# Optimization experiments

Measured on AMD Instinct MI355X. Metric: run time of the kernel, lower is better.

The kernel has to match this reference:

```python
import math
import jax, jax.numpy as jnp
import numpy as np
from jax import lax

B, T, D, S, N_SLOTS, N_ITERS = 16, 4096, 768, 768, 16, 8
THR, EPS = 0.5, 1e-8
SCALE = D ** -0.5
NEG = -jnp.finfo(jnp.float32).max


def ln(x, g, b):
    mu = x.mean(-1, keepdims=True)
    var = ((x - mu) ** 2).mean(-1, keepdims=True)
    return (x - mu) / jnp.sqrt(var + 1e-5) * g + b


def gru_cell(u, h, wih, whh, bih, bhh):
    # torch GRUCell: r,z,n gate ordering
    gi = u @ wih.T + bih
    gh = h @ whh.T + bhh
    ir, iz, inn = jnp.split(gi, 3, axis=-1)
    hr, hz, hn = jnp.split(gh, 3, axis=-1)
    r = jax.nn.sigmoid(ir + hr)
    z = jax.nn.sigmoid(iz + hz)
    n = jnp.tanh(inn + r * hn)
    return (1.0 - z) * n + z * h


def sa_step(slots, k, v, p, slot_mask, context_mask):
    q = ln(slots, p['lsg'], p['lsb']) @ p['Wq'].T
    dots = jnp.einsum('bid,bjd->bij', q, k) * SCALE  # [B, n_slots, T]
    dots = jnp.where(context_mask[:, None, :], dots, NEG)
    if slot_mask is not None:
        dots = jnp.where(slot_mask[:, :, None], dots, NEG)
    attn_vis = jax.nn.softmax(dots, axis=1)  # softmax over SLOTS (inverted attn)
    attn = attn_vis + EPS
    attn = attn / attn.sum(-1, keepdims=True)
    updates = jnp.einsum('bjd,bij->bid', v, attn)
    b, n, d = slots.shape
    h = gru_cell(updates.reshape(b * n, d), slots.reshape(b * n, d),
                 p['gwih'], p['gwhh'], p['gbih'], p['gbhh'])
    slots = h.reshape(b, n, d)
    pre = ln(slots, p['lfg'], p['lfb'])
    slots = slots + (jax.nn.relu(pre @ p['w1'].T + p['b1']) @ p['w2'].T + p['b2'])
    return slots, attn_vis


def cluster_single(slots, attn, slot_mask):
    sl = lax.stop_gradient(slots)  # torch no_grad block
    ns = sl / jnp.clip(jnp.linalg.norm(sl, axis=-1, keepdims=True), 1e-12)
    smm = (slot_mask[:, :, None] & slot_mask[:, None, :]).astype(jnp.float32)
    dist = 1.0 - jnp.einsum('bnd,bmd->bnm', ns, ns)
    dist = jnp.where(smm > 0, dist, 2.0)
    adj = (dist < THR).astype(jnp.float32) * smm
    for _ in range(math.ceil(math.log2(N_SLOTS))):  # transitive closure by squaring
        adj = jnp.minimum(adj @ adj, 1.0) * smm
    cum = jnp.cumsum(adj, axis=1)
    cm = adj * (cum <= 1.0)  # keep first row of each connected component
    counts = (cm > 0).any(axis=2).sum(axis=1)
    reset = counts < 3
    eye = jnp.eye(N_SLOTS, dtype=jnp.float32)[None] * slot_mask[:, :, None].astype(jnp.float32)
    cm = jnp.where(reset[:, None, None], eye, cm)
    cw = cm / jnp.clip(cm.sum(axis=2, keepdims=True), 1.0)
    cm = lax.stop_gradient(cm)
    cw = lax.stop_gradient(cw)
    means = cw @ slots          # grads flow through slots only
    cattn = cm @ attn           # grads flow through attn only
    out_mask = (cm > 0).any(axis=2) & slot_mask
    return means, cattn, out_mask


def setup_inputs() -> dict:
    key = jax.random.key(0)
    ks = jax.random.split(key, 16)
    sc = 0.02
    return {
        'x': jax.random.normal(ks[0], (B, T, D), jnp.float32),
        'context_mask': jnp.ones((B, T), jnp.bool_),
        'n_slots': N_SLOTS,
        'slots_init': jax.random.normal(ks[1], (N_SLOTS, S), jnp.float32),
        'Wk': jax.random.normal(ks[2], (S, D), jnp.float32) * sc,
        'Wv': jax.random.normal(ks[3], (S, D), jnp.float32) * sc,
        'Wq': jax.random.normal(ks[4], (S, S), jnp.float32) * sc,
        'gwih': jax.random.normal(ks[5], (3 * S, S), jnp.float32) * sc,
        'gwhh': jax.random.normal(ks[6], (3 * S, S), jnp.float32) * sc,
        'gbih': jnp.zeros((3 * S,), jnp.float32),
        'gbhh': jnp.zeros((3 * S,), jnp.float32),
        'w1': jax.random.normal(ks[7], (4 * S, S), jnp.float32) * sc,
        'b1': jnp.zeros((4 * S,), jnp.float32),
        'w2': jax.random.normal(ks[8], (S, 4 * S), jnp.float32) * sc,
        'b2': jnp.zeros((S,), jnp.float32),
        'lin_g': jnp.ones((D,), jnp.float32), 'lin_b': jnp.zeros((D,), jnp.float32),
        'lsg': jnp.ones((S,), jnp.float32), 'lsb': jnp.zeros((S,), jnp.float32),
        'lfg': jnp.ones((S,), jnp.float32), 'lfb': jnp.zeros((S,), jnp.float32),
    }


def reference(x, context_mask, n_slots, slots_init, Wk, Wv, Wq, gwih, gwhh,
              gbih, gbhh, w1, b1, w2, b2, lin_g, lin_b, lsg, lsb, lfg, lfb):
    p = dict(Wq=Wq, gwih=gwih, gwhh=gwhh, gbih=gbih, gbhh=gbhh,
             w1=w1, b1=b1, w2=w2, b2=b2, lsg=lsg, lsb=lsb, lfg=lfg, lfb=lfb)
    xn = ln(x, lin_g, lin_b)
    init_slots = jnp.broadcast_to(slots_init[None], (x.shape[0], N_SLOTS, S))
    k = xn @ Wk.T
    v = xn @ Wv.T
    slots = init_slots
    for _ in range(N_ITERS):
        slots, attn = sa_step(slots, k, v, p, None, context_mask)
    # implicit differentiation trick
    slots = lax.stop_gradient(slots) - lax.stop_gradient(init_slots) + init_slots
    slot_mask = jnp.ones((x.shape[0], N_SLOTS), jnp.bool_)
    slots, attn = sa_step(slots, k, v, p, slot_mask, context_mask)
    slots, attn, slot_mask = cluster_single(slots, attn, slot_mask)
    attn_map = jnp.transpose(attn, (0, 2, 1))  # [B, T, n_slots]
    return slots, attn_map, slot_mask
```

## Files before the change

kernel.cpp:

```cpp
#include <hip/hip_runtime.h>
#include <hip/hip_bf16.h>

typedef __hip_bfloat16 bf16;
typedef __attribute__((ext_vector_type(4))) float f32x4;
typedef __attribute__((ext_vector_type(8))) short s16x8;
typedef unsigned int u32;
typedef unsigned short u16;

#define B_ 16
#define T_ 4096
#define D_ 768
#define S_ 768
#define NS 16
#define NIT 9
#define NCHUNK 16
#define TCH 256
#define EPS 1e-8f
#define SCALE 0.036084391824351615f

__device__ __forceinline__ void gld16(const void* g, void* l) {
    __builtin_amdgcn_global_load_lds((const __attribute__((address_space(1))) u32*)g,
                                     (__attribute__((address_space(3))) u32*)l, 16, 0, 0);
}

__device__ __forceinline__ u16 bfbits(float x) {
    bf16 h = __float2bfloat16(x);
    return *reinterpret_cast<u16*>(&h);
}

__global__ void f2bf_kernel(const float* __restrict__ in, bf16* __restrict__ out, int n) {
    int i = blockIdx.x * 256 + threadIdx.x;
    if (i < n) out[i] = __float2bfloat16(in[i]);
}

__global__ void __launch_bounds__(256) ln768_kernel(
    const float* __restrict__ x, const float* __restrict__ g,
    const float* __restrict__ bta, bf16* __restrict__ out)
{
    int row = blockIdx.x;
    int tid = threadIdx.x;
    const float* xr = x + (size_t)row * 768;
    float v0 = xr[tid], v1 = xr[tid + 256], v2 = xr[tid + 512];
    float s = v0 + v1 + v2;
    int lane = tid & 63, wid = tid >> 6;
    #pragma unroll
    for (int off = 32; off; off >>= 1) s += __shfl_down(s, off);
    __shared__ float red[4];
    __shared__ float sh_mu, sh_rs;
    if (lane == 0) red[wid] = s;
    __syncthreads();
    if (tid == 0) sh_mu = (red[0] + red[1] + red[2] + red[3]) * (1.f / 768.f);
    __syncthreads();
    float mu = sh_mu;
    float d0 = v0 - mu, d1 = v1 - mu, d2 = v2 - mu;
    float q = d0 * d0 + d1 * d1 + d2 * d2;
    #pragma unroll
    for (int off = 32; off; off >>= 1) q += __shfl_down(q, off);
    if (lane == 0) red[wid] = q;
    __syncthreads();
    if (tid == 0) sh_rs = rsqrtf((red[0] + red[1] + red[2] + red[3]) * (1.f / 768.f) + 1e-5f);
    __syncthreads();
    float rs = sh_rs;
    bf16* orow = out + (size_t)row * 768;
    orow[tid]       = __float2bfloat16(d0 * rs * g[tid]       + bta[tid]);
    orow[tid + 256] = __float2bfloat16(d1 * rs * g[tid + 256] + bta[tid + 256]);
    orow[tid + 512] = __float2bfloat16(d2 * rs * g[tid + 512] + bta[tid + 512]);
}

__global__ void __launch_bounds__(256) gemm128_kernel(
    const bf16* __restrict__ A, const bf16* __restrict__ Bm, bf16* __restrict__ Cb,
    int M, int N, int K)
{
    __shared__ bf16 As[128 * 64];
    __shared__ bf16 Bs[128 * 64];
    int tid = threadIdx.x, lane = tid & 63, wid = tid >> 6;
    int bm0 = blockIdx.x * 128, bn0 = blockIdx.y * 128;
    int wr = wid >> 1, wc = wid & 1;
    int g = lane >> 4, r15 = lane & 15;
    const f32x4 vzero = {0.f, 0.f, 0.f, 0.f};
    f32x4 acc[4][4];
    #pragma unroll
    for (int m = 0; m < 4; ++m)
        #pragma unroll
        for (int n = 0; n < 4; ++n) acc[m][n] = vzero;

    for (int kt = 0; kt < K; kt += 64) {
        __syncthreads();
        #pragma unroll
        for (int i = 0; i < 4; ++i) {
            int sa = wid * 64 + i * 256;
            int o = (sa + lane) * 16;
            int r = o >> 7, cb = o & 127;
            int cbs = cb ^ ((r & 7) << 4);
            gld16(A + (size_t)(bm0 + r) * K + kt + (cbs >> 1), (char*)As + (size_t)sa * 16);
        }
        #pragma unroll
        for (int i = 0; i < 4; ++i) {
            int sa = wid * 64 + i * 256;
            int o = (sa + lane) * 16;
            int r = o >> 7, cb = o & 127;
            int cbs = cb ^ ((r & 7) << 4);
            gld16(Bm + (size_t)(bn0 + r) * K + kt + (cbs >> 1), (char*)Bs + (size_t)sa * 16);
        }
        asm volatile("s_waitcnt vmcnt(0)" ::: "memory");
        __syncthreads();
        #pragma unroll
        for (int kk = 0; kk < 64; kk += 32) {
            s16x8 af[4], bfr[4];
            #pragma unroll
            for (int m = 0; m < 4; ++m) {
                int r = wr * 64 + m * 16 + r15;
                int p = r * 128 + ((kk * 2 + g * 16) ^ ((r & 7) << 4));
                af[m] = *(const s16x8*)((const char*)As + p);
            }
            #pragma unroll
            for (int n = 0; n < 4; ++n) {
                int r = wc * 64 + n * 16 + r15;
                int p = r * 128 + ((kk * 2 + g * 16) ^ ((r & 7) << 4));
                bfr[n] = *(const s16x8*)((const char*)Bs + p);
            }
            #pragma unroll
            for (int m = 0; m < 4; ++m)
                #pragma unroll
                for (int n = 0; n < 4; ++n)
                    acc[m][n] = __builtin_amdgcn_mfma_f32_16x16x32_bf16(af[m], bfr[n], acc[m][n], 0, 0, 0);
        }
    }
    #pragma unroll
    for (int m = 0; m < 4; ++m) {
        int cm = bm0 + wr * 64 + m * 16 + g * 4;
        #pragma unroll
        for (int n = 0; n < 4; ++n) {
            int cn = bn0 + wc * 64 + n * 16 + r15;
            #pragma unroll
            for (int j = 0; j < 4; ++j)
                Cb[(size_t)(cm + j) * N + cn] = __float2bfloat16(acc[m][n][j]);
        }
    }
}

__global__ void __launch_bounds__(256) gemm_skinny_kernel(
    const bf16* __restrict__ A, const bf16* __restrict__ Bm,
    const float* __restrict__ bias, float* __restrict__ Cf, bf16* __restrict__ Cb,
    int M, int N, int K, int relu, int addC)
{
    __shared__ bf16 As[16 * 64];
    __shared__ bf16 Bs[64 * 64];
    int tid = threadIdx.x, lane = tid & 63, wid = tid >> 6;
    int bm0 = blockIdx.x * 16, bn0 = blockIdx.y * 64;
    int g = lane >> 4, r15 = lane & 15;
    const f32x4 vzero = {0.f, 0.f, 0.f, 0.f};
    f32x4 acc = vzero;
    for (int kt = 0; kt < K; kt += 64) {
        __syncthreads();
        #pragma unroll
        for (int i = 0; i < 3; ++i) {
            int s0 = i * 256 + wid * 64;
            if (s0 < 640) {
                int o = (s0 + lane) * 16;
                if (o < 2048) {
                    int r = o >> 7, cb = o & 127;
                    int cbs = cb ^ ((r & 7) << 4);
                    gld16(A + (size_t)(bm0 + r) * K + kt + (cbs >> 1), (char*)As + (size_t)s0 * 16);
                } else {
                    int ob = o - 2048;
                    int r = ob >> 7, cb = ob & 127;
                    int cbs = cb ^ ((r & 7) << 4);
                    gld16(Bm + (size_t)(bn0 + r) * K + kt + (cbs >> 1),
                          (char*)Bs + (size_t)(s0 * 16 - 2048));
                }
            }
        }
        asm volatile("s_waitcnt vmcnt(0)" ::: "memory");
        __syncthreads();
        #pragma unroll
        for (int kk = 0; kk < 64; kk += 32) {
            int ra = r15;
            int pa = ra * 128 + ((kk * 2 + g * 16) ^ ((ra & 7) << 4));
            s16x8 af = *(const s16x8*)((const char*)As + pa);
            int rb = wid * 16 + r15;
            int pb = rb * 128 + ((kk * 2 + g * 16) ^ ((rb & 7) << 4));
            s16x8 bfr = *(const s16x8*)((const char*)Bs + pb);
            acc = __builtin_amdgcn_mfma_f32_16x16x32_bf16(af, bfr, acc, 0, 0, 0);
        }
    }
    int cn = bn0 + wid * 16 + r15;
    float bv = bias ? bias[cn] : 0.f;
    #pragma unroll
    for (int j = 0; j < 4; ++j) {
        int cm = bm0 + g * 4 + j;
        size_t ci = (size_t)cm * N + cn;
        float val = acc[j] + bv;
        if (addC) val += Cf[ci];
        if (relu) val = fmaxf(val, 0.f);
        if (Cf) Cf[ci] = val;
        if (Cb) Cb[ci] = __float2bfloat16(val);
    }
}

__global__ void __launch_bounds__(256) transpose_kernel(
    const bf16* __restrict__ v, bf16* __restrict__ vt)
{
    __shared__ bf16 tile[32][33];
    int b = blockIdx.z;
    int t0 = blockIdx.x * 32, d0 = blockIdx.y * 32;
    int tx = threadIdx.x & 31, ty = threadIdx.x >> 5;
    const bf16* vb = v + (size_t)b * T_ * S_;
    bf16* vtb = vt + (size_t)b * S_ * T_;
    #pragma unroll
    for (int r = ty; r < 32; r += 8)
        tile[r][tx] = vb[(size_t)(t0 + r) * S_ + d0 + tx];
    __syncthreads();
    #pragma unroll
    for (int r = ty; r < 32; r += 8)
        vtb[(size_t)(d0 + r) * T_ + t0 + tx] = tile[tx][r];
}

__global__ void __launch_bounds__(256) vsum_kernel(
    const bf16* __restrict__ vT, float* __restrict__ vsum)
{
    int row = blockIdx.x * 4 + (threadIdx.x >> 6);
    int lane = threadIdx.x & 63;
    const bf16* p = vT + (size_t)row * T_;
    float s = 0.f;
    for (int t = lane * 8; t < T_; t += 64 * 8) {
        s16x8 v8 = *(const s16x8*)(p + t);
        #pragma unroll
        for (int j = 0; j < 8; ++j) {
            union { u32 i; float f; } c;
            c.i = ((u32)(u16)v8[j]) << 16;
            s += c.f;
        }
    }
    #pragma unroll
    for (int off = 32; off; off >>= 1) s += __shfl_down(s, off);
    if (lane == 0) vsum[row] = s;
}

__global__ void init_slots_kernel(const float* __restrict__ si,
                                  float* __restrict__ slots, bf16* __restrict__ slots_bf)
{
    int idx = blockIdx.x * 256 + threadIdx.x;
    float v = si[idx % (NS * S_)];
    slots[idx] = v;
    slots_bf[idx] = __float2bfloat16(v);
}

__global__ void __launch_bounds__(256) fused_attn_kernel(
    const bf16* __restrict__ q_bf, const bf16* __restrict__ k_bf, const bf16* __restrict__ vT,
    float* __restrict__ pU, float* __restrict__ prs, float* __restrict__ avis, int write_avis)
{
    __shared__ bf16 qs[16 * 768];
    __shared__ bf16 ks[32 * 768];
    __shared__ bf16 vs[768 * 32];
    __shared__ bf16 as_[16 * 32];
    __shared__ float rsw[2][16];
    int tid = threadIdx.x, lane = tid & 63, wid = tid >> 6;
    int b = blockIdx.x >> 4, chunk = blockIdx.x & 15;
    int t0 = chunk * TCH;
    int g = lane >> 4, s15 = lane & 15;
    const bf16* qb  = q_bf + (size_t)(b * 16) * 768;
    const bf16* kb  = k_bf + (size_t)b * T_ * 768;
    const bf16* vtb = vT   + (size_t)b * 768 * T_;

    #pragma unroll
    for (int i = 0; i < 6; ++i) {
        int s0 = i * 256 + wid * 64;
        int o = (s0 + lane) * 16;
        int r = o / 1536, cb = o % 1536;
        int cbs = cb ^ ((r & 7) << 4);
        gld16(qb + (size_t)r * 768 + (cbs >> 1), (char*)qs + (size_t)s0 * 16);
    }

    const f32x4 vzero = {0.f, 0.f, 0.f, 0.f};
    f32x4 uacc[12];
    #pragma unroll
    for (int i = 0; i < 12; ++i) uacc[i] = vzero;
    float rs_acc = 0.f;

    for (int ts = 0; ts < TCH / 32; ++ts) {
        int tb = t0 + ts * 32;
        __syncthreads();
        #pragma unroll
        for (int i = 0; i < 12; ++i) {
            int s0 = i * 256 + wid * 64;
            int o = (s0 + lane) * 16;
            int r = o / 1536, cb = o % 1536;
            int cbs = cb ^ ((r & 7) << 4);
            gld16(kb + (size_t)(tb + r) * 768 + (cbs >> 1), (char*)ks + (size_t)s0 * 16);
        }
        #pragma unroll
        for (int i = 0; i < 12; ++i) {
            int s0 = i * 256 + wid * 64;
            int o = (s0 + lane) * 16;
            int d = o >> 6, cb = o & 63;
            int cbs = cb ^ ((d & 3) << 4);
            gld16(vtb + (size_t)d * T_ + tb + (cbs >> 1), (char*)vs + (size_t)s0 * 16);
        }
        asm volatile("s_waitcnt vmcnt(0)" ::: "memory");
        __syncthreads();

        if (wid < 2) {
            f32x4 dacc = vzero;
            #pragma unroll
            for (int kk = 0; kk < 768; kk += 32) {
                int rk = wid * 16 + s15;
                int pk = rk * 1536 + ((kk * 2 + g * 16) ^ ((rk & 7) << 4));
                s16x8 kf = *(const s16x8*)((const char*)ks + pk);
                int pq = s15 * 1536 + ((kk * 2 + g * 16) ^ ((s15 & 7) << 4));
                s16x8 qf = *(const s16x8*)((const char*)qs + pq);
                dacc = __builtin_amdgcn_mfma_f32_16x16x32_bf16(kf, qf, dacc, 0, 0, 0);
            }
            float d0 = dacc[0] * SCALE, d1 = dacc[1] * SCALE,
                  d2 = dacc[2] * SCALE, d3 = dacc[3] * SCALE;
            float m0 = d0, m1 = d1, m2 = d2, m3 = d3;
            #pragma unroll
            for (int off = 1; off < 16; off <<= 1) {
                m0 = fmaxf(m0, __shfl_xor(m0, off));
                m1 = fmaxf(m1, __shfl_xor(m1, off));
                m2 = fmaxf(m2, __shfl_xor(m2, off));
                m3 = fmaxf(m3, __shfl_xor(m3, off));
            }
            float e0 = expf(d0 - m0), e1 = expf(d1 - m1), e2 = expf(d2 - m2), e3 = expf(d3 - m3);
            float q0 = e0, q1 = e1, q2 = e2, q3 = e3;
            #pragma unroll
            for (int off = 1; off < 16; off <<= 1) {
                q0 += __shfl_xor(q0, off);
                q1 += __shfl_xor(q1, off);
                q2 += __shfl_xor(q2, off);
                q3 += __shfl_xor(q3, off);
            }
            float a0 = e0 / q0, a1 = e1 / q1, a2 = e2 / q2, a3 = e3 / q3;
            rs_acc += a0 + a1 + a2 + a3;
            int tl = wid * 16 + g * 4;
            ushort2 p0, p1;
            p0.x = bfbits(a0); p0.y = bfbits(a1);
            p1.x = bfbits(a2); p1.y = bfbits(a3);
            int sw = (s15 & 3) << 4;
            *(ushort2*)((char*)as_ + s15 * 64 + ((tl * 2) ^ sw))       = p0;
            *(ushort2*)((char*)as_ + s15 * 64 + (((tl + 2) * 2) ^ sw)) = p1;
            if (write_avis) {
                f32x4 w = {a0, a1, a2, a3};
                *(f32x4*)(avis + (size_t)(b * 16 + s15) * T_ + tb + tl) = w;
            }
        }
        __syncthreads();
        {
            int pa = s15 * 64 + ((g * 16) ^ ((s15 & 3) << 4));
            s16x8 afr = *(const s16x8*)((const char*)as_ + pa);
            #pragma unroll
            for (int i = 0; i < 12; ++i) {
                int d = (wid * 12 + i) * 16 + s15;
                int pv = d * 64 + ((g * 16) ^ ((d & 3) << 4));
                s16x8 vf = *(const s16x8*)((const char*)vs + pv);
                uacc[i] = __builtin_amdgcn_mfma_f32_16x16x32_bf16(vf, afr, uacc[i], 0, 0, 0);
            }
        }
    }
    float* pUb = pU + (size_t)(b * 16 + chunk) * 768 * 16;
    #pragma unroll
    for (int i = 0; i < 12; ++i) {
        int dbase = (wid * 12 + i) * 16 + g * 4;
        #pragma unroll
        for (int j = 0; j < 4; ++j)
            pUb[(size_t)(dbase + j) * 16 + s15] = uacc[i][j];
    }
    rs_acc += __shfl_xor(rs_acc, 16);
    rs_acc += __shfl_xor(rs_acc, 32);
    if (wid < 2 && lane < 16) rsw[wid][s15] = rs_acc;
    __syncthreads();
    if (tid < 16) prs[(b * 16 + chunk) * 16 + tid] = rsw[0][tid] + rsw[1][tid];
}

__global__ void __launch_bounds__(256) attn_reduce_kernel(
    const float* __restrict__ pU, const float* __restrict__ prs,
    const float* __restrict__ vsum, bf16* __restrict__ upd)
{
    int idx = blockIdx.x * 256 + threadIdx.x;
    int d = idx % 768;
    int s = (idx / 768) & 15;
    int b = idx / (768 * 16);
    float su = 0.f;
    #pragma unroll
    for (int c = 0; c < 16; ++c) su += pU[((size_t)(b * 16 + c) * 768 + d) * 16 + s];
    float rs = 0.f;
    #pragma unroll
    for (int c = 0; c < 16; ++c) rs += prs[(b * 16 + c) * 16 + s];
    float val = (su + EPS * vsum[b * 768 + d]) / (rs + T_ * EPS);
    upd[idx] = __float2bfloat16(val);
}

__global__ void __launch_bounds__(256) gru_gates_kernel(
    const float* __restrict__ gi, const float* __restrict__ gh,
    float* __restrict__ slots, bf16* __restrict__ slots_bf)
{
    int idx = blockIdx.x * 256 + threadIdx.x;
    int r = idx / 768, c = idx - r * 768;
    const float* gir = gi + (size_t)r * 2304;
    const float* ghr = gh + (size_t)r * 2304;
    float ir = gir[c], iz = gir[768 + c], inn = gir[1536 + c];
    float hr = ghr[c], hz = ghr[768 + c], hn  = ghr[1536 + c];
    float rg = 1.f / (1.f + expf(-(ir + hr)));
    float z  = 1.f / (1.f + expf(-(iz + hz)));
    float n  = tanhf(inn + rg * hn);
    float h  = slots[idx];
    float out = (1.f - z) * n + z * h;
    slots[idx] = out;
    slots_bf[idx] = __float2bfloat16(out);
}

__global__ void __launch_bounds__(256) cluster_kernel(
    const float* __restrict__ slots, float* __restrict__ out_slots,
    float* __restrict__ out_mask, float* __restrict__ cm_g)
{
    int b = blockIdx.x;
    __shared__ float s[16][768];
    __shared__ float inv[16];
    __shared__ float adj[16][16], tmp[16][16], cw[16][16];
    __shared__ int reset_s;
    const float* sb = slots + (size_t)b * 16 * 768;
    for (int i = threadIdx.x; i < 16 * 768; i += 256) s[i / 768][i % 768] = sb[i];
    __syncthreads();
    if (threadIdx.x < 16) {
        float q = 0.f;
        for (int d = 0; d < 768; ++d) q += s[threadIdx.x][d] * s[threadIdx.x][d];
        inv[threadIdx.x] = 1.f / fmaxf(sqrtf(q), 1e-12f);
    }
    __syncthreads();
    int n = threadIdx.x >> 4, m = threadIdx.x & 15;
    float dot = 0.f;
    for (int d = 0; d < 768; ++d) dot += s[n][d] * s[m][d];
    dot *= inv[n] * inv[m];
    adj[n][m] = ((1.f - dot) < 0.5f) ? 1.f : 0.f;
    __syncthreads();
    #pragma unroll
    for (int it = 0; it < 4; ++it) {
        float t = 0.f;
        #pragma unroll
        for (int j = 0; j < 16; ++j) t += adj[n][j] * adj[j][m];
        tmp[n][m] = fminf(t, 1.f);
        __syncthreads();
// ... 59 lines not shown
        for (int j = 0; j < 16; ++j) acc += cm[i][j] * avv[j];
        out_attn[((size_t)b * T_ + t) * 16 + i] = acc;
    }
}

extern "C" void kernel_launch(void* const* d_in, const int* in_sizes, int n_in,
                              void* d_out, int out_size, void* d_ws, size_t ws_size,
                              hipStream_t stream)
{
    const float* x    = (const float*)d_in[0];
    const float* si   = (const float*)d_in[3];
    const float* Wk   = (const float*)d_in[4];
    const float* Wv   = (const float*)d_in[5];
    const float* Wq   = (const float*)d_in[6];
    const float* gwih = (const float*)d_in[7];
    const float* gwhh = (const float*)d_in[8];
    const float* gbih = (const float*)d_in[9];
    const float* gbhh = (const float*)d_in[10];
    const float* w1   = (const float*)d_in[11];
    const float* b1   = (const float*)d_in[12];
    const float* w2   = (const float*)d_in[13];
    const float* b2   = (const float*)d_in[14];
    const float* ling = (const float*)d_in[15];
    const float* linb = (const float*)d_in[16];
    const float* lsg  = (const float*)d_in[17];
    const float* lsb  = (const float*)d_in[18];
    const float* lfg  = (const float*)d_in[19];
    const float* lfb  = (const float*)d_in[20];

    char* w = (char*)d_ws;
    size_t off = 0;
    auto alloc = [&](size_t bytes) { void* p = w + off; off += (bytes + 255) & ~(size_t)255; return p; };
    bf16* xn_vt  = (bf16*)alloc((size_t)B_ * T_ * D_ * 2);
    bf16* k_bf   = (bf16*)alloc((size_t)B_ * T_ * S_ * 2);
    bf16* v_bf   = (bf16*)alloc((size_t)B_ * T_ * S_ * 2);
    float* avis  = (float*)alloc((size_t)B_ * NS * T_ * 4);
    float* pU    = (float*)alloc((size_t)B_ * NCHUNK * S_ * NS * 4);
    float* prs   = (float*)alloc((size_t)B_ * NCHUNK * NS * 4);
    float* vsum  = (float*)alloc((size_t)B_ * S_ * 4);
    float* slots = (float*)alloc((size_t)B_ * NS * S_ * 4);
    bf16* slots_bf = (bf16*)alloc((size_t)B_ * NS * S_ * 2);
    bf16* lnsl   = (bf16*)alloc((size_t)B_ * NS * S_ * 2);
    bf16* q_bf   = (bf16*)alloc((size_t)B_ * NS * S_ * 2);
    bf16* upd_bf = (bf16*)alloc((size_t)B_ * NS * S_ * 2);
    float* gi    = (float*)alloc((size_t)B_ * NS * 3 * S_ * 4);
    float* gh    = (float*)alloc((size_t)B_ * NS * 3 * S_ * 4);
    bf16* h1_bf  = (bf16*)alloc((size_t)B_ * NS * 4 * S_ * 2);
    bf16* wq_bf  = (bf16*)alloc((size_t)S_ * S_ * 2);
    bf16* wk_bf  = (bf16*)alloc((size_t)S_ * D_ * 2);
    bf16* wv_bf  = (bf16*)alloc((size_t)S_ * D_ * 2);
    bf16* gwih_bf = (bf16*)alloc((size_t)3 * S_ * S_ * 2);
    bf16* gwhh_bf = (bf16*)alloc((size_t)3 * S_ * S_ * 2);
    bf16* w1_bf  = (bf16*)alloc((size_t)4 * S_ * S_ * 2);
    bf16* w2_bf  = (bf16*)alloc((size_t)S_ * 4 * S_ * 2);
    float* cm_g  = (float*)alloc((size_t)B_ * 256 * 4);

    float* out_slots = (float*)d_out;
    float* out_attn  = out_slots + (size_t)B_ * NS * S_;
    float* out_mask  = out_attn + (size_t)B_ * T_ * NS;

    auto cvt = [&](const float* src, bf16* dst, int n) {
        f2bf_kernel<<<(n + 255) / 256, 256, 0, stream>>>(src, dst, n);
    };
    cvt(Wq, wq_bf, S_ * S_);
    cvt(Wk, wk_bf, S_ * D_);
    cvt(Wv, wv_bf, S_ * D_);
    cvt(gwih, gwih_bf, 3 * S_ * S_);
    cvt(gwhh, gwhh_bf, 3 * S_ * S_);
    cvt(w1, w1_bf, 4 * S_ * S_);
    cvt(w2, w2_bf, S_ * 4 * S_);

    ln768_kernel<<<B_ * T_, 256, 0, stream>>>(x, ling, linb, xn_vt);

    {
        dim3 g(B_ * T_ / 128, S_ / 128);
        gemm128_kernel<<<g, 256, 0, stream>>>(xn_vt, wk_bf, k_bf, B_ * T_, S_, D_);
        gemm128_kernel<<<g, 256, 0, stream>>>(xn_vt, wv_bf, v_bf, B_ * T_, S_, D_);
    }
    {
        dim3 g(T_ / 32, S_ / 32, B_);
        transpose_kernel<<<g, 256, 0, stream>>>(v_bf, xn_vt);
    }
    bf16* vT = xn_vt;
    vsum_kernel<<<B_ * S_ / 4, 256, 0, stream>>>(vT, vsum);

    init_slots_kernel<<<(B_ * NS * S_) / 256, 256, 0, stream>>>(si, slots, slots_bf);

    for (int it = 0; it < NIT; ++it) {
        ln768_kernel<<<B_ * NS, 256, 0, stream>>>(slots, lsg, lsb, lnsl);
        {
            dim3 g(B_ * NS / 16, S_ / 64);
            gemm_skinny_kernel<<<g, 256, 0, stream>>>(lnsl, wq_bf, nullptr, nullptr, q_bf,
                                                      B_ * NS, S_, S_, 0, 0);
        }
        fused_attn_kernel<<<B_ * NCHUNK, 256, 0, stream>>>(q_bf, k_bf, vT, pU, prs, avis,
                                                           (it == NIT - 1) ? 1 : 0);
        attn_reduce_kernel<<<(B_ * NS * S_) / 256, 256, 0, stream>>>(pU, prs, vsum, upd_bf);
        {
            dim3 g(B_ * NS / 16, 3 * S_ / 64);
            gemm_skinny_kernel<<<g, 256, 0, stream>>>(upd_bf, gwih_bf, gbih, gi, nullptr,
                                                      B_ * NS, 3 * S_, S_, 0, 0);
            gemm_skinny_kernel<<<g, 256, 0, stream>>>(slots_bf, gwhh_bf, gbhh, gh, nullptr,
                                                      B_ * NS, 3 * S_, S_, 0, 0);
        }
        gru_gates_kernel<<<(B_ * NS * S_) / 256, 256, 0, stream>>>(gi, gh, slots, slots_bf);
        ln768_kernel<<<B_ * NS, 256, 0, stream>>>(slots, lfg, lfb, lnsl);
        {
            dim3 g(B_ * NS / 16, 4 * S_ / 64);
            gemm_skinny_kernel<<<g, 256, 0, stream>>>(lnsl, w1_bf, b1, nullptr, h1_bf,
                                                      B_ * NS, 4 * S_, S_, 1, 0);
        }
        {
            dim3 g(B_ * NS / 16, S_ / 64);
            gemm_skinny_kernel<<<g, 256, 0, stream>>>(h1_bf, w2_bf, b2, slots, slots_bf,
                                                      B_ * NS, S_, 4 * S_, 0, 1);
        }
    }

    cluster_kernel<<<B_, 256, 0, stream>>>(slots, out_slots, out_mask, cm_g);
    {
        dim3 g(T_ / 256, B_);
        cattn_kernel<<<g, 256, 0, stream>>>(avis, cm_g, out_attn);
    }
}
```

Before: 1.669 ms.

## Fuse slot-update kernels, merge K/V projection, double-buffer big GEMM

Several unrelated changes land together. The seven weight conversions become one launch, and K and V are computed by a single GEMM into an interleaved buffer. That GEMM now uses double-buffered LDS and a swapped grid order. The V transpose is fused with the column sum through atomics. In the iteration loop, LayerNorm is fused into the Q and MLP-up GEMMs, the GRU input/hidden GEMMs are fused with the gate math, and the MLP-down GEMM is fused with the residual add, with ping-pong slot buffers. The attention kernel now reads K and Q straight from global memory instead of staging them in LDS. The aim is fewer launches and less intermediate traffic, at the cost of uncached global weight reads and more register pressure.

```diff
diff --git a/kernel.cpp b/kernel.cpp
--- a/kernel.cpp
+++ b/kernel.cpp
@@ -28,9 +28,29 @@
     return *reinterpret_cast<u16*>(&h);
 }
 
-__global__ void f2bf_kernel(const float* __restrict__ in, bf16* __restrict__ out, int n) {
+__global__ void __launch_bounds__(256) cvt_all_kernel(
+    const float* __restrict__ wq, const float* __restrict__ wk, const float* __restrict__ wv,
+    const float* __restrict__ gwih, const float* __restrict__ gwhh,
+    const float* __restrict__ w1, const float* __restrict__ w2,
+    bf16* __restrict__ wq_b, bf16* __restrict__ wkv_b,
+    bf16* __restrict__ gwih_b, bf16* __restrict__ gwhh_b,
+    bf16* __restrict__ w1_b, bf16* __restrict__ w2_b)
+{
     int i = blockIdx.x * 256 + threadIdx.x;
-    if (i < n) out[i] = __float2bfloat16(in[i]);
+    const int NW = 589824, NG = 1769472, NM = 2359296;
+    if (i < NW) { wq_b[i] = __float2bfloat16(wq[i]); return; }
+    i -= NW;
+    if (i < NW) { wkv_b[i] = __float2bfloat16(wk[i]); return; }
+    i -= NW;
+    if (i < NW) { wkv_b[NW + i] = __float2bfloat16(wv[i]); return; }
+    i -= NW;
+    if (i < NG) { gwih_b[i] = __float2bfloat16(gwih[i]); return; }
+    i -= NG;
+    if (i < NG) { gwhh_b[i] = __float2bfloat16(gwhh[i]); return; }
+    i -= NG;
+    if (i < NM) { w1_b[i] = __float2bfloat16(w1[i]); return; }
+    i -= NM;
+    w2_b[i] = __float2bfloat16(w2[i]);
 }
 
 __global__ void __launch_bounds__(256) ln768_kernel(
@@ -71,10 +91,10 @@
     const bf16* __restrict__ A, const bf16* __restrict__ Bm, bf16* __restrict__ Cb,
     int M, int N, int K)
 {
-    __shared__ bf16 As[128 * 64];
-    __shared__ bf16 Bs[128 * 64];
+    __shared__ bf16 As[2][128 * 64];
+    __shared__ bf16 Bs[2][128 * 64];
     int tid = threadIdx.x, lane = tid & 63, wid = tid >> 6;
-    int bm0 = blockIdx.x * 128, bn0 = blockIdx.y * 128;
+    int bm0 = blockIdx.y * 128, bn0 = blockIdx.x * 128;
     int wr = wid >> 1, wc = wid & 1;
     int g = lane >> 4, r15 = lane & 15;
     const f32x4 vzero = {0.f, 0.f, 0.f, 0.f};
@@ -84,15 +104,15 @@
         #pragma unroll
         for (int n = 0; n < 4; ++n) acc[m][n] = vzero;
 
-    for (int kt = 0; kt < K; kt += 64) {
-        __syncthreads();
+    auto stage = [&](int buf, int kt) {
         #pragma unroll
         for (int i = 0; i < 4; ++i) {
             int sa = wid * 64 + i * 256;
             int o = (sa + lane) * 16;
             int r = o >> 7, cb = o & 127;
             int cbs = cb ^ ((r & 7) << 4);
-            gld16(A + (size_t)(bm0 + r) * K + kt + (cbs >> 1), (char*)As + (size_t)sa * 16);
+            gld16(A + (size_t)(bm0 + r) * K + kt + (cbs >> 1),
+                  (char*)As[buf] + (size_t)sa * 16);
         }
         #pragma unroll
         for (int i = 0; i < 4; ++i) {
@@ -100,10 +120,18 @@
             int o = (sa + lane) * 16;
             int r = o >> 7, cb = o & 127;
             int cbs = cb ^ ((r & 7) << 4);
-            gld16(Bm + (size_t)(bn0 + r) * K + kt + (cbs >> 1), (char*)Bs + (size_t)sa * 16);
-        }
-        asm volatile("s_waitcnt vmcnt(0)" ::: "memory");
-        __syncthreads();
+            gld16(Bm + (size_t)(bn0 + r) * K + kt + (cbs >> 1),
+                  (char*)Bs[buf] + (size_t)sa * 16);
+        }
+    };
+
+    stage(0, 0);
+    asm volatile("s_waitcnt vmcnt(0)" ::: "memory");
+    __syncthreads();
+    int nk = K / 64;
+    for (int t = 0; t < nk; ++t) {
+        int cur = t & 1;
+        if (t + 1 < nk) stage(cur ^ 1, (t + 1) * 64);
         #pragma unroll
         for (int kk = 0; kk < 64; kk += 32) {
             s16x8 af[4], bfr[4];
@@ -111,13 +139,13 @@
             for (int m = 0; m < 4; ++m) {
                 int r = wr * 64 + m * 16 + r15;
                 int p = r * 128 + ((kk * 2 + g * 16) ^ ((r & 7) << 4));
-                af[m] = *(const s16x8*)((const char*)As + p);
+                af[m] = *(const s16x8*)((const char*)As[cur] + p);
             }
             #pragma unroll
             for (int n = 0; n < 4; ++n) {
                 int r = wc * 64 + n * 16 + r15;
                 int p = r * 128 + ((kk * 2 + g * 16) ^ ((r & 7) << 4));
-                bfr[n] = *(const s16x8*)((const char*)Bs + p);
+                bfr[n] = *(const s16x8*)((const char*)Bs[cur] + p);
             }
             #pragma unroll
             for (int m = 0; m < 4; ++m)
@@ -125,6 +153,8 @@
                 for (int n = 0; n < 4; ++n)
                     acc[m][n] = __builtin_amdgcn_mfma_f32_16x16x32_bf16(af[m], bfr[n], acc[m][n], 0, 0, 0);
         }
+        asm volatile("s_waitcnt vmcnt(0)" ::: "memory");
+        __syncthreads();
     }
     #pragma unroll
     for (int m = 0; m < 4; ++m) {
@@ -139,102 +169,28 @@
     }
 }
 
-__global__ void __launch_bounds__(256) gemm_skinny_kernel(
-    const bf16* __restrict__ A, const bf16* __restrict__ Bm,
-    const float* __restrict__ bias, float* __restrict__ Cf, bf16* __restrict__ Cb,
-    int M, int N, int K, int relu, int addC)
-{
-    __shared__ bf16 As[16 * 64];
-    __shared__ bf16 Bs[64 * 64];
-    int tid = threadIdx.x, lane = tid & 63, wid = tid >> 6;
-    int bm0 = blockIdx.x * 16, bn0 = blockIdx.y * 64;
-    int g = lane >> 4, r15 = lane & 15;
-    const f32x4 vzero = {0.f, 0.f, 0.f, 0.f};
-    f32x4 acc = vzero;
-    for (int kt = 0; kt < K; kt += 64) {
-        __syncthreads();
-        #pragma unroll
-        for (int i = 0; i < 3; ++i) {
-            int s0 = i * 256 + wid * 64;
-            if (s0 < 640) {
-                int o = (s0 + lane) * 16;
-                if (o < 2048) {
-                    int r = o >> 7, cb = o & 127;
-                    int cbs = cb ^ ((r & 7) << 4);
-                    gld16(A + (size_t)(bm0 + r) * K + kt + (cbs >> 1), (char*)As + (size_t)s0 * 16);
-                } else {
-                    int ob = o - 2048;
-                    int r = ob >> 7, cb = ob & 127;
-                    int cbs = cb ^ ((r & 7) << 4);
-                    gld16(Bm + (size_t)(bn0 + r) * K + kt + (cbs >> 1),
-                          (char*)Bs + (size_t)(s0 * 16 - 2048));
-                }
-            }
-        }
-        asm volatile("s_waitcnt vmcnt(0)" ::: "memory");
-        __syncthreads();
-        #pragma unroll
-        for (int kk = 0; kk < 64; kk += 32) {
-            int ra = r15;
-            int pa = ra * 128 + ((kk * 2 + g * 16) ^ ((ra & 7) << 4));
-            s16x8 af = *(const s16x8*)((const char*)As + pa);
-            int rb = wid * 16 + r15;
-            int pb = rb * 128 + ((kk * 2 + g * 16) ^ ((rb & 7) << 4));
-            s16x8 bfr = *(const s16x8*)((const char*)Bs + pb);
-            acc = __builtin_amdgcn_mfma_f32_16x16x32_bf16(af, bfr, acc, 0, 0, 0);
-        }
-    }
-    int cn = bn0 + wid * 16 + r15;
-    float bv = bias ? bias[cn] : 0.f;
-    #pragma unroll
-    for (int j = 0; j < 4; ++j) {
-        int cm = bm0 + g * 4 + j;
-        size_t ci = (size_t)cm * N + cn;
-        float val = acc[j] + bv;
-        if (addC) val += Cf[ci];
-        if (relu) val = fmaxf(val, 0.f);
-        if (Cf) Cf[ci] = val;
-        if (Cb) Cb[ci] = __float2bfloat16(val);
-    }
-}
-
-__global__ void __launch_bounds__(256) transpose_kernel(
-    const bf16* __restrict__ v, bf16* __restrict__ vt)
+__global__ void __launch_bounds__(256) transpose_vsum_kernel(
+    const bf16* __restrict__ kv, bf16* __restrict__ vt, float* __restrict__ vsum)
 {
     __shared__ bf16 tile[32][33];
     int b = blockIdx.z;
     int t0 = blockIdx.x * 32, d0 = blockIdx.y * 32;
     int tx = threadIdx.x & 31, ty = threadIdx.x >> 5;
-    const bf16* vb = v + (size_t)b * T_ * S_;
+    const bf16* vb = kv + (size_t)b * T_ * 1536 + 768;
     bf16* vtb = vt + (size_t)b * S_ * T_;
     #pragma unroll
     for (int r = ty; r < 32; r += 8)
-        tile[r][tx] = vb[(size_t)(t0 + r) * S_ + d0 + tx];
+        tile[r][tx] = vb[(size_t)(t0 + r) * 1536 + d0 + tx];
     __syncthreads();
     #pragma unroll
     for (int r = ty; r < 32; r += 8)
         vtb[(size_t)(d0 + r) * T_ + t0 + tx] = tile[tx][r];
-}
-
-__global__ void __launch_bounds__(256) vsum_kernel(
-    const bf16* __restrict__ vT, float* __restrict__ vsum)
-{
-    int row = blockIdx.x * 4 + (threadIdx.x >> 6);
-    int lane = threadIdx.x & 63;
-    const bf16* p = vT + (size_t)row * T_;
-    float s = 0.f;
-    for (int t = lane * 8; t < T_; t += 64 * 8) {
-        s16x8 v8 = *(const s16x8*)(p + t);
-        #pragma unroll
-        for (int j = 0; j < 8; ++j) {
-            union { u32 i; float f; } c;
-            c.i = ((u32)(u16)v8[j]) << 16;
-            s += c.f;
-        }
-    }
-    #pragma unroll
-    for (int off = 32; off; off >>= 1) s += __shfl_down(s, off);
-    if (lane == 0) vsum[row] = s;
+    if (threadIdx.x < 32) {
+        float s = 0.f;
+        #pragma unroll
+        for (int r = 0; r < 32; ++r) s += __bfloat162float(tile[r][threadIdx.x]);
+        atomicAdd(vsum + b * 768 + d0 + threadIdx.x, s);
+    }
 }
 
 __global__ void init_slots_kernel(const float* __restrict__ si,
@@ -246,116 +202,124 @@
     slots_bf[idx] = __float2bfloat16(v);
 }
 
+__global__ void __launch_bounds__(256) ln_gemm_kernel(
+    const float* __restrict__ xin, const float* __restrict__ gam, const float* __restrict__ bet,
+    const bf16* __restrict__ W, const float* __restrict__ bias,
+    bf16* __restrict__ out, int N, int relu)
+{
+    __shared__ bf16 As[16 * 768];
+    int tid = threadIdx.x;
+    int bx = blockIdx.x, bn0 = blockIdx.y * 64;
+    int row = tid >> 4, li = tid & 15;
+    const float* xr = xin + (size_t)(bx * 16 + row) * 768;
+    float vals[48];
+    float s = 0.f;
+    #pragma unroll
+    for (int i = 0; i < 48; ++i) { vals[i] = xr[li + i * 16]; s += vals[i]; }
+    #pragma unroll
+    for (int m = 1; m < 16; m <<= 1) s += __shfl_xor(s, m);
+    float mu = s * (1.f / 768.f);
+    float q = 0.f;
+    #pragma unroll
+    for (int i = 0; i < 48; ++i) { float d = vals[i] - mu; q += d * d; }
+    #pragma unroll
+    for (int m = 1; m < 16; m <<= 1) q += __shfl_xor(q, m);
+    float rs = rsqrtf(q * (1.f / 768.f) + 1e-5f);
+    #pragma unroll
+    for (int i = 0; i < 48; ++i) {
+        int c = li + i * 16;
+        float v = (vals[i] - mu) * rs * gam[c] + bet[c];
+        *(u16*)((char*)As + row * 1536 + ((c * 2) ^ ((row & 7) << 4))) = bfbits(v);
+    }
+    __syncthreads();
+    int lane = tid & 63, wid = tid >> 6;
+    int g = lane >> 4, s15 = lane & 15;
+    int cn = bn0 + wid * 16 + s15;
+    f32x4 acc = {0.f, 0.f, 0.f, 0.f};
+    for (int kk = 0; kk < 768; kk += 32) {
+        s16x8 af = *(const s16x8*)((const char*)As + s15 * 1536 + ((kk * 2 + g * 16) ^ ((s15 & 7) << 4)));
+        s16x8 bf_ = *(const s16x8*)(W + (size_t)cn * 768 + kk + g * 8);
+        acc = __builtin_amdgcn_mfma_f32_16x16x32_bf16(af, bf_, acc, 0, 0, 0);
+    }
+    float bv = bias ? bias[cn] : 0.f;
+    #pragma unroll
+    for (int j = 0; j < 4; ++j) {
+        float val = acc[j] + bv;
+        if (relu) val = fmaxf(val, 0.f);
+        out[(size_t)(bx * 16 + g * 4 + j) * N + cn] = __float2bfloat16(val);
+    }
+}
+
 __global__ void __launch_bounds__(256) fused_attn_kernel(
-    const bf16* __restrict__ q_bf, const bf16* __restrict__ k_bf, const bf16* __restrict__ vT,
+    const bf16* __restrict__ q_bf, const bf16* __restrict__ kv, const bf16* __restrict__ vT,
     float* __restrict__ pU, float* __restrict__ prs, float* __restrict__ avis, int write_avis)
 {
-    __shared__ bf16 qs[16 * 768];
-    __shared__ bf16 ks[32 * 768];
-    __shared__ bf16 vs[768 * 32];
-    __shared__ bf16 as_[16 * 32];
-    __shared__ float rsw[2][16];
+    __shared__ bf16 as_[16 * 64];
+    __shared__ float rsw[4][16];
     int tid = threadIdx.x, lane = tid & 63, wid = tid >> 6;
     int b = blockIdx.x >> 4, chunk = blockIdx.x & 15;
     int t0 = chunk * TCH;
     int g = lane >> 4, s15 = lane & 15;
-    const bf16* qb  = q_bf + (size_t)(b * 16) * 768;
-    const bf16* kb  = k_bf + (size_t)b * T_ * 768;
-    const bf16* vtb = vT   + (size_t)b * 768 * T_;
-
-    #pragma unroll
-    for (int i = 0; i < 6; ++i) {
-        int s0 = i * 256 + wid * 64;
-        int o = (s0 + lane) * 16;
-        int r = o / 1536, cb = o % 1536;
-        int cbs = cb ^ ((r & 7) << 4);
-        gld16(qb + (size_t)r * 768 + (cbs >> 1), (char*)qs + (size_t)s0 * 16);
-    }
-
+    const bf16* qb  = q_bf + (size_t)b * 16 * 768;
+    const bf16* kb  = kv + (size_t)b * T_ * 1536;
+    const bf16* vtb = vT + (size_t)b * 768 * T_;
     const f32x4 vzero = {0.f, 0.f, 0.f, 0.f};
     f32x4 uacc[12];
     #pragma unroll
     for (int i = 0; i < 12; ++i) uacc[i] = vzero;
     float rs_acc = 0.f;
 
-    for (int ts = 0; ts < TCH / 32; ++ts) {
-        int tb = t0 + ts * 32;
+    for (int w4 = 0; w4 < 4; ++w4) {
+        int tb = t0 + w4 * 64;
+        int trow = tb + wid * 16 + s15;
+        f32x4 dacc = vzero;
+        #pragma unroll
+        for (int kk = 0; kk < 768; kk += 32) {
+            s16x8 kf = *(const s16x8*)(kb + (size_t)trow * 1536 + kk + g * 8);
+            s16x8 qf = *(const s16x8*)(qb + (size_t)s15 * 768 + kk + g * 8);
+            dacc = __builtin_amdgcn_mfma_f32_16x16x32_bf16(kf, qf, dacc, 0, 0, 0);
+        }
+        float d0 = dacc[0] * SCALE, d1 = dacc[1] * SCALE,
+              d2 = dacc[2] * SCALE, d3 = dacc[3] * SCALE;
+        float m0 = d0, m1 = d1, m2 = d2, m3 = d3;
+        #pragma unroll
+        for (int off = 1; off < 16; off <<= 1) {
+            m0 = fmaxf(m0, __shfl_xor(m0, off));
+            m1 = fmaxf(m1, __shfl_xor(m1, off));
+            m2 = fmaxf(m2, __shfl_xor(m2, off));
+            m3 = fmaxf(m3, __shfl_xor(m3, off));
+        }
+        float e0 = expf(d0 - m0), e1 = expf(d1 - m1), e2 = expf(d2 - m2), e3 = expf(d3 - m3);
+        float q0 = e0, q1 = e1, q2 = e2, q3 = e3;
+        #pragma unroll
+        for (int off = 1; off < 16; off <<= 1) {
+            q0 += __shfl_xor(q0, off);
+            q1 += __shfl_xor(q1, off);
+            q2 += __shfl_xor(q2, off);
+            q3 += __shfl_xor(q3, off);
+        }
+        float a0 = e0 / q0, a1 = e1 / q1, a2 = e2 / q2, a3 = e3 / q3;
+        rs_acc += a0 + a1 + a2 + a3;
+        u32 p01 = (u32)bfbits(a0) | ((u32)bfbits(a1) << 16);
+        u32 p23 = (u32)bfbits(a2) | ((u32)bfbits(a3) << 16);
+        uint2 pk; pk.x = p01; pk.y = p23;
+        *(uint2*)((char*)as_ + s15 * 128 + ((wid * 32 + g * 8) ^ ((s15 & 7) << 4))) = pk;
+        if (write_avis) {
+            f32x4 w = {a0, a1, a2, a3};
+            *(f32x4*)(avis + (size_t)(b * 16 + s15) * T_ + tb + wid * 16 + g * 4) = w;
+        }
         __syncthreads();
         #pragma unroll
-        for (int i = 0; i < 12; ++i) {
-            int s0 = i * 256 + wid * 64;
-            int o = (s0 + lane) * 16;
-            int r = o / 1536, cb = o % 1536;
-            int cbs = cb ^ ((r & 7) << 4);
-            gld16(kb + (size_t)(tb + r) * 768 + (cbs >> 1), (char*)ks + (size_t)s0 * 16);
-        }
-        #pragma unroll
-        for (int i = 0; i < 12; ++i) {
-            int s0 = i * 256 + wid * 64;
-            int o = (s0 + lane) * 16;
-            int d = o >> 6, cb = o & 63;
-            int cbs = cb ^ ((d & 3) << 4);
-            gld16(vtb + (size_t)d * T_ + tb + (cbs >> 1), (char*)vs + (size_t)s0 * 16);
-        }
-        asm volatile("s_waitcnt vmcnt(0)" ::: "memory");
-        __syncthreads();
-
-        if (wid < 2) {
-            f32x4 dacc = vzero;
-            #pragma unroll
-            for (int kk = 0; kk < 768; kk += 32) {
-                int rk = wid * 16 + s15;
-                int pk = rk * 1536 + ((kk * 2 + g * 16) ^ ((rk & 7) << 4));
-                s16x8 kf = *(const s16x8*)((const char*)ks + pk);
-                int pq = s15 * 1536 + ((kk * 2 + g * 16) ^ ((s15 & 7) << 4));
-                s16x8 qf = *(const s16x8*)((const char*)qs + pq);
-                dacc = __builtin_amdgcn_mfma_f32_16x16x32_bf16(kf, qf, dacc, 0, 0, 0);
-            }
-            float d0 = dacc[0] * SCALE, d1 = dacc[1] * SCALE,
-                  d2 = dacc[2] * SCALE, d3 = dacc[3] * SCALE;
-            float m0 = d0, m1 = d1, m2 = d2, m3 = d3;
-            #pragma unroll
-            for (int off = 1; off < 16; off <<= 1) {
-                m0 = fmaxf(m0, __shfl_xor(m0, off));
-                m1 = fmaxf(m1, __shfl_xor(m1, off));
-                m2 = fmaxf(m2, __shfl_xor(m2, off));
-                m3 = fmaxf(m3, __shfl_xor(m3, off));
-            }
-            float e0 = expf(d0 - m0), e1 = expf(d1 - m1), e2 = expf(d2 - m2), e3 = expf(d3 - m3);
-            float q0 = e0, q1 = e1, q2 = e2, q3 = e3;
-            #pragma unroll
-            for (int off = 1; off < 16; off <<= 1) {
-                q0 += __shfl_xor(q0, off);
-                q1 += __shfl_xor(q1, off);
-                q2 += __shfl_xor(q2, off);
-                q3 += __shfl_xor(q3, off);
-            }
-            float a0 = e0 / q0, a1 = e1 / q1, a2 = e2 / q2, a3 = e3 / q3;
-            rs_acc += a0 + a1 + a2 + a3;
-            int tl = wid * 16 + g * 4;
-            ushort2 p0, p1;
-            p0.x = bfbits(a0); p0.y = bfbits(a1);
-            p1.x = bfbits(a2); p1.y = bfbits(a3);
-            int sw = (s15 & 3) << 4;
-            *(ushort2*)((char*)as_ + s15 * 64 + ((tl * 2) ^ sw))       = p0;
-            *(ushort2*)((char*)as_ + s15 * 64 + (((tl + 2) * 2) ^ sw)) = p1;
-            if (write_avis) {
-                f32x4 w = {a0, a1, a2, a3};
-                *(f32x4*)(avis + (size_t)(b * 16 + s15) * T_ + tb + tl) = w;
-            }
-        }
-        __syncthreads();
-        {
-            int pa = s15 * 64 + ((g * 16) ^ ((s15 & 3) << 4));
-            s16x8 afr = *(const s16x8*)((const char*)as_ + pa);
+        for (int ks = 0; ks < 2; ++ks) {
+            s16x8 af = *(const s16x8*)((const char*)as_ + s15 * 128 + ((ks * 64 + g * 16) ^ ((s15 & 7) << 4)));
             #pragma unroll
             for (int i = 0; i < 12; ++i) {
                 int d = (wid * 12 + i) * 16 + s15;
-                int pv = d * 64 + ((g * 16) ^ ((d & 3) << 4));
-                s16x8 vf = *(const s16x8*)((const char*)vs + pv);
-                uacc[i] = __builtin_amdgcn_mfma_f32_16x16x32_bf16(vf, afr, uacc[i], 0, 0, 0);
+                s16x8 vf = *(const s16x8*)(vtb + (size_t)d * T_ + tb + ks * 32 + g * 8);
+                uacc[i] = __builtin_amdgcn_mfma_f32_16x16x32_bf16(vf, af, uacc[i], 0, 0, 0);
             }
         }
+        __syncthreads();
     }
     float* pUb = pU + (size_t)(b * 16 + chunk) * 768 * 16;
     #pragma unroll
@@ -367,9 +331,10 @@
     }
     rs_acc += __shfl_xor(rs_acc, 16);
     rs_acc += __shfl_xor(rs_acc, 32);
-    if (wid < 2 && lane < 16) rsw[wid][s15] = rs_acc;
-    __syncthreads();
-    if (tid < 16) prs[(b * 16 + chunk) * 16 + tid] = rsw[0][tid] + rsw[1][tid];
+    if (lane < 16) rsw[wid][s15] = rs_acc;
+    __syncthreads();
+    if (tid < 16)
+        prs[(b * 16 + chunk) * 16 + tid] = rsw[0][tid] + rsw[1][tid] + rsw[2][tid] + rsw[3][tid];
 }
 
 __global__ void __launch_bounds__(256) attn_reduce_kernel(
@@ -390,23 +355,77 @@
     upd[idx] = __float2bfloat16(val);
 }
 
-__global__ void __launch_bounds__(256) gru_gates_kernel(
-    const float* __restrict__ gi, const float* __restrict__ gh,
-    float* __restrict__ slots, bf16* __restrict__ slots_bf)
-{
-    int idx = blockIdx.x * 256 + threadIdx.x;
-    int r = idx / 768, c = idx - r * 768;
-    const float* gir = gi + (size_t)r * 2304;
-    const float* ghr = gh + (size_t)r * 2304;
-    float ir = gir[c], iz = gir[768 + c], inn = gir[1536 + c];
-    float hr = ghr[c], hz = ghr[768 + c], hn  = ghr[1536 + c];
-    float rg = 1.f / (1.f + expf(-(ir + hr)));
-    float z  = 1.f / (1.f + expf(-(iz + hz)));
-    float n  = tanhf(inn + rg * hn);
-    float h  = slots[idx];
-    float out = (1.f - z) * n + z * h;
-    slots[idx] = out;
-    slots_bf[idx] = __float2bfloat16(out);
+__global__ void __launch_bounds__(256) fused_gru_kernel(
+    const bf16* __restrict__ upd, const bf16* __restrict__ slots_bf,
+    const bf16* __restrict__ Wih, const bf16* __restrict__ Whh,
+    const float* __restrict__ bih, const float* __restrict__ bhh,
+    const float* __restrict__ slots_f, float* __restrict__ slots_out)
+{
+    int tid = threadIdx.x, lane = tid & 63, wid = tid >> 6;
+    int bx = blockIdx.x, c0 = blockIdx.y * 64;
+    int g = lane >> 4, s15 = lane & 15;
+    int cn = c0 + wid * 16 + s15;
+    const f32x4 vz = {0.f, 0.f, 0.f, 0.f};
+    f32x4 air = vz, aiz = vz, ain = vz, ahr = vz, ahz = vz, ahn = vz;
+    const bf16* au_b = upd + (size_t)(bx * 16 + s15) * 768;
+    const bf16* ah_b = slots_bf + (size_t)(bx * 16 + s15) * 768;
+    const bf16* wr_ = Wih + (size_t)cn * 768;
+    const bf16* wz_ = Wih + (size_t)(768 + cn) * 768;
+    const bf16* wn_ = Wih + (size_t)(1536 + cn) * 768;
+    const bf16* vr_ = Whh + (size_t)cn * 768;
+    const bf16* vz_ = Whh + (size_t)(768 + cn) * 768;
+    const bf16* vn_ = Whh + (size_t)(1536 + cn) * 768;
+    for (int kk = 0; kk < 768; kk += 32) {
+        int ko = kk + g * 8;
+        s16x8 au = *(const s16x8*)(au_b + ko);
+        s16x8 ah = *(const s16x8*)(ah_b + ko);
+        air = __builtin_amdgcn_mfma_f32_16x16x32_bf16(au, *(const s16x8*)(wr_ + ko), air, 0, 0, 0);
+        aiz = __builtin_amdgcn_mfma_f32_16x16x32_bf16(au, *(const s16x8*)(wz_ + ko), aiz, 0, 0, 0);
+        ain = __builtin_amdgcn_mfma_f32_16x16x32_bf16(au, *(const s16x8*)(wn_ + ko), ain, 0, 0, 0);
+        ahr = __builtin_amdgcn_mfma_f32_16x16x32_bf16(ah, *(const s16x8*)(vr_ + ko), ahr, 0, 0, 0);
+        ahz = __builtin_amdgcn_mfma_f32_16x16x32_bf16(ah, *(const s16x8*)(vz_ + ko), ahz, 0, 0, 0);
+        ahn = __builtin_amdgcn_mfma_f32_16x16x32_bf16(ah, *(const s16x8*)(vn_ + ko), ahn, 0, 0, 0);
+    }
+    float bir = bih[cn], biz = bih[768 + cn], bin_ = bih[1536 + cn];
+    float bhr = bhh[cn], bhz = bhh[768 + cn], bhn = bhh[1536 + cn];
+    #pragma unroll
+    for (int j = 0; j < 4; ++j) {
+        int m = bx * 16 + g * 4 + j;
+        float ir = air[j] + bir, iz = aiz[j] + biz, inn = ain[j] + bin_;
+        float hr = ahr[j] + bhr, hz = ahz[j] + bhz, hn = ahn[j] + bhn;
+        float r = 1.f / (1.f + expf(-(ir + hr)));
+        float z = 1.f / (1.f + expf(-(iz + hz)));
+        float n = tanhf(inn + r * hn);
+        float h = slots_f[(size_t)m * 768 + cn];
+        slots_out[(size_t)m * 768 + cn] = (1.f - z) * n + z * h;
+    }
+}
+
+__global__ void __launch_bounds__(256) mlp_out_kernel(
+    const bf16* __restrict__ h1, const bf16* __restrict__ W2,
+    const float* __restrict__ b2, const float* __restrict__ slots_in,
+    float* __restrict__ slots_f, bf16* __restrict__ slots_b)
+{
+    int tid = threadIdx.x, lane = tid & 63, wid = tid >> 6;
+    int bx = blockIdx.x, c0 = blockIdx.y * 64;
+    int g = lane >> 4, s15 = lane & 15;
+    int cn = c0 + wid * 16 + s15;
+    const bf16* a_b = h1 + (size_t)(bx * 16 + s15) * 3072;
+    const bf16* w_b = W2 + (size_t)cn * 3072;
+    f32x4 acc = {0.f, 0.f, 0.f, 0.f};
+    for (int kk = 0; kk < 3072; kk += 32) {
+        s16x8 af = *(const s16x8*)(a_b + kk + g * 8);
+        s16x8 bf_ = *(const s16x8*)(w_b + kk + g * 8);
+        acc = __builtin_amdgcn_mfma_f32_16x16x32_bf16(af, bf_, acc, 0, 0, 0);
+    }
+    float bv = b2[cn];
+    #pragma unroll
+    for (int j = 0; j < 4; ++j) {
+        int m = bx * 16 + g * 4 + j;
+        float val = acc[j] + bv + slots_in[(size_t)m * 768 + cn];
+        slots_f[(size_t)m * 768 + cn] = val;
+        slots_b[(size_t)m * 768 + cn] = __float2bfloat16(val);
+    }
 }
 
 __global__ void __launch_bounds__(256) cluster_kernel(
@@ -532,23 +551,19 @@
     size_t off = 0;
     auto alloc = [&](size_t bytes) { void* p = w + off; off += (bytes + 255) & ~(size_t)255; return p; };
     bf16* xn_vt  = (bf16*)alloc((size_t)B_ * T_ * D_ * 2);
-    bf16* k_bf   = (bf16*)alloc((size_t)B_ * T_ * S_ * 2);
-    bf16* v_bf   = (bf16*)alloc((size_t)B_ * T_ * S_ * 2);
+    bf16* kv     = (bf16*)alloc((size_t)B_ * T_ * 1536 * 2);
     float* avis  = (float*)alloc((size_t)B_ * NS * T_ * 4);
     float* pU    = (float*)alloc((size_t)B_ * NCHUNK * S_ * NS * 4);
     float* prs   = (float*)alloc((size_t)B_ * NCHUNK * NS * 4);
     float* vsum  = (float*)alloc((size_t)B_ * S_ * 4);
-    float* slots = (float*)alloc((size_t)B_ * NS * S_ * 4);
-    bf16* slots_bf = (bf16*)alloc((size_t)B_ * NS * S_ * 2);
-    bf16* lnsl   = (bf16*)alloc((size_t)B_ * NS * S_ * 2);
+    float* slotsA = (float*)alloc((size_t)B_ * NS * S_ * 4);
+    bf16* slotsA_bf = (bf16*)alloc((size_t)B_ * NS * S_ * 2);
+    float* slotsB = (float*)alloc((size_t)B_ * NS * S_ * 4);
     bf16* q_bf   = (bf16*)alloc((size_t)B_ * NS * S_ * 2);
     bf16* upd_bf = (bf16*)alloc((size_t)B_ * NS * S_ * 2);
-    float* gi    = (float*)alloc((size_t)B_ * NS * 3 * S_ * 4);
-    float* gh    = (float*)alloc((size_t)B_ * NS * 3 * S_ * 4);
     bf16* h1_bf  = (bf16*)alloc((size_t)B_ * NS * 4 * S_ * 2);
     bf16* wq_bf  = (bf16*)alloc((size_t)S_ * S_ * 2);
-    bf16* wk_bf  = (bf16*)alloc((size_t)S_ * D_ * 2);
-    bf16* wv_bf  = (bf16*)alloc((size_t)S_ * D_ * 2);
+    bf16* wkv_bf = (bf16*)alloc((size_t)1536 * D_ * 2);
     bf16* gwih_bf = (bf16*)alloc((size_t)3 * S_ * S_ * 2);
     bf16* gwhh_bf = (bf16*)alloc((size_t)3 * S_ * S_ * 2);
     bf16* w1_bf  = (bf16*)alloc((size_t)4 * S_ * S_ * 2);
@@ -559,65 +574,52 @@
     float* out_attn  = out_slots + (size_t)B_ * NS * S_;
     float* out_mask  = out_attn + (size_t)B_ * T_ * NS;
 
-    auto cvt = [&](const float* src, bf16* dst, int n) {
-        f2bf_kernel<<<(n + 255) / 256, 256, 0, stream>>>(src, dst, n);
-    };
-    cvt(Wq, wq_bf, S_ * S_);
-    cvt(Wk, wk_bf, S_ * D_);
-    cvt(Wv, wv_bf, S_ * D_);
-    cvt(gwih, gwih_bf, 3 * S_ * S_);
-    cvt(gwhh, gwhh_bf, 3 * S_ * S_);
-    cvt(w1, w1_bf, 4 * S_ * S_);
-    cvt(w2, w2_bf, S_ * 4 * S_);
+    cvt_all_kernel<<<39168, 256, 0, stream>>>(Wq, Wk, Wv, gwih, gwhh, w1, w2,
+                                              wq_bf, wkv_bf, gwih_bf, gwhh_bf, w1_bf, w2_bf);
 
     ln768_kernel<<<B_ * T_, 256, 0, stream>>>(x, ling, linb, xn_vt);
 
     {
-        dim3 g(B_ * T_ / 128, S_ / 128);
-        gemm128_kernel<<<g, 256, 0, stream>>>(xn_vt, wk_bf, k_bf, B_ * T_, S_, D_);
-        gemm128_kernel<<<g, 256, 0, stream>>>(xn_vt, wv_bf, v_bf, B_ * T_, S_, D_);
-    }
+        dim3 g(1536 / 128, B_ * T_ / 128);
+        gemm128_kernel<<<g, 256, 0, stream>>>(xn_vt, wkv_bf, kv, B_ * T_, 1536, D_);
+    }
+
+    hipMemsetAsync(vsum, 0, (size_t)B_ * S_ * 4, stream);
     {
         dim3 g(T_ / 32, S_ / 32, B_);
-        transpose_kernel<<<g, 256, 0, stream>>>(v_bf, xn_vt);
+        transpose_vsum_kernel<<<g, 256, 0, stream>>>(kv, xn_vt, vsum);
     }
     bf16* vT = xn_vt;
-    vsum_kernel<<<B_ * S_ / 4, 256, 0, stream>>>(vT, vsum);
-
-    init_slots_kernel<<<(B_ * NS * S_) / 256, 256, 0, stream>>>(si, slots, slots_bf);
+
+    init_slots_kernel<<<(B_ * NS * S_) / 256, 256, 0, stream>>>(si, slotsA, slotsA_bf);
 
     for (int it = 0; it < NIT; ++it) {
-        ln768_kernel<<<B_ * NS, 256, 0, stream>>>(slots, lsg, lsb, lnsl);
         {
-            dim3 g(B_ * NS / 16, S_ / 64);
-            gemm_skinny_kernel<<<g, 256, 0, stream>>>(lnsl, wq_bf, nullptr, nullptr, q_bf,
-                                                      B_ * NS, S_, S_, 0, 0);
-        }
-        fused_attn_kernel<<<B_ * NCHUNK, 256, 0, stream>>>(q_bf, k_bf, vT, pU, prs, avis,
+            dim3 g(16, 12);
+            ln_gemm_kernel<<<g, 256, 0, stream>>>(slotsA, lsg, lsb, wq_bf, nullptr,
+                                                  q_bf, 768, 0);
+        }
+        fused_attn_kernel<<<B_ * NCHUNK, 256, 0, stream>>>(q_bf, kv, vT, pU, prs, avis,
                                                            (it == NIT - 1) ? 1 : 0);
         attn_reduce_kernel<<<(B_ * NS * S_) / 256, 256, 0, stream>>>(pU, prs, vsum, upd_bf);
         {
-            dim3 g(B_ * NS / 16, 3 * S_ / 64);
-            gemm_skinny_kernel<<<g, 256, 0, stream>>>(upd_bf, gwih_bf, gbih, gi, nullptr,
-                                                      B_ * NS, 3 * S_, S_, 0, 0);
-            gemm_skinny_kernel<<<g, 256, 0, stream>>>(slots_bf, gwhh_bf, gbhh, gh, nullptr,
-                                                      B_ * NS, 3 * S_, S_, 0, 0);
-        }
-        gru_gates_kernel<<<(B_ * NS * S_) / 256, 256, 0, stream>>>(gi, gh, slots, slots_bf);
-        ln768_kernel<<<B_ * NS, 256, 0, stream>>>(slots, lfg, lfb, lnsl);
+            dim3 g(16, 12);
+            fused_gru_kernel<<<g, 256, 0, stream>>>(upd_bf, slotsA_bf, gwih_bf, gwhh_bf,
+                                                    gbih, gbhh, slotsA, slotsB);
+        }
         {
-            dim3 g(B_ * NS / 16, 4 * S_ / 64);
-            gemm_skinny_kernel<<<g, 256, 0, stream>>>(lnsl, w1_bf, b1, nullptr, h1_bf,
-                                                      B_ * NS, 4 * S_, S_, 1, 0);
+            dim3 g(16, 48);
+            ln_gemm_kernel<<<g, 256, 0, stream>>>(slotsB, lfg, lfb, w1_bf, b1,
+                                                  h1_bf, 3072, 1);
         }
         {
-            dim3 g(B_ * NS / 16, S_ / 64);
-            gemm_skinny_kernel<<<g, 256, 0, stream>>>(h1_bf, w2_bf, b2, slots, slots_bf,
-                                                      B_ * NS, S_, 4 * S_, 0, 1);
-        }
-    }
-
-    cluster_kernel<<<B_, 256, 0, stream>>>(slots, out_slots, out_mask, cm_g);
+            dim3 g(16, 12);
+            mlp_out_kernel<<<g, 256, 0, stream>>>(h1_bf, w2_bf, b2, slotsB,
+                                                  slotsA, slotsA_bf);
+        }
+    }
+
+    cluster_kernel<<<B_, 256, 0, stream>>>(slotsA, out_slots, out_mask, cm_g);
     {
         dim3 g(T_ / 256, B_);
         cattn_kernel<<<g, 256, 0, stream>>>(avis, cm_g, out_attn);
```

After: 2.093 ms. 1.25x slower.
